# Kernel optimization log

Measured on AMD Instinct MI355X. Metric: run time of the kernel, lower is better.

Reference implementation:

```python
import jax, jax.numpy as jnp
import numpy as np

B, S, E, H, NE, K = 4, 1024, 1024, 16, 8, 2
DFF = 4 * E
DH = E // H
EPS = 1e-5


def _ln(x, g, b):
    m = jnp.mean(x, axis=-1, keepdims=True)
    v = jnp.mean(jnp.square(x - m), axis=-1, keepdims=True)
    return (x - m) * jax.lax.rsqrt(v + EPS) * g + b


def setup_inputs() -> dict:
    key = jax.random.key(0)
    ks = jax.random.split(key, 20)
    n = lambda k, sh, s: (jax.random.normal(k, sh, jnp.float32) * s)
    return {
        'x': n(ks[0], (B, S, E), 1.0),
        'ln1_g': jnp.ones((E,), jnp.float32), 'ln1_b': jnp.zeros((E,), jnp.float32),
        'wq': n(ks[1], (E, E), 0.02), 'bq': jnp.zeros((E,), jnp.float32),
        'wk': n(ks[2], (E, E), 0.02), 'bk': jnp.zeros((E,), jnp.float32),
        'wv': n(ks[3], (E, E), 0.02), 'bv': jnp.zeros((E,), jnp.float32),
        'wo': n(ks[4], (E, E), 0.02), 'bo': jnp.zeros((E,), jnp.float32),
        'ln2_g': jnp.ones((E,), jnp.float32), 'ln2_b': jnp.zeros((E,), jnp.float32),
        'sw1': n(ks[5], (E, DFF), 0.02), 'sb1': jnp.zeros((DFF,), jnp.float32),
        'sw2': n(ks[6], (DFF, E), 0.02), 'sb2': jnp.zeros((E,), jnp.float32),
        'ew1': n(ks[7], (NE, E, DFF), 0.02), 'eb1': jnp.zeros((NE, DFF), jnp.float32),
        'ew2': n(ks[8], (NE, DFF, E), 0.02), 'eb2': jnp.zeros((NE, E), jnp.float32),
        'w_gate': n(ks[9], (E, NE), 1.0),
    }


def reference(x, ln1_g, ln1_b, wq, bq, wk, bk, wv, bv, wo, bo,
              ln2_g, ln2_b, sw1, sb1, sw2, sb2, ew1, eb1, ew2, eb2, w_gate):
    # --- self-attention sublayer (eval: no dropout) ---
    res1 = x
    h = _ln(x, ln1_g, ln1_b)
    q = (h @ wq + bq).reshape(B, S, H, DH)
    k = (h @ wk + bk).reshape(B, S, H, DH)
    v = (h @ wv + bv).reshape(B, S, H, DH)
    scores = jnp.einsum('bqhd,bkhd->bhqk', q, k) / jnp.sqrt(jnp.float32(DH))
    attn = jax.nn.softmax(scores, axis=-1)
    ctx = jnp.einsum('bhqk,bkhd->bqhd', attn, v).reshape(B, S, E)
    x = res1 + (ctx @ wo + bo)

    # --- MoE sublayer ---
    res2 = x
    h2 = _ln(x, ln2_g, ln2_b)
    shared = jax.nn.gelu(h2 @ sw1 + sb1, approximate=False) @ sw2 + sb2

    # router (eval: clean logits, no noise)
    logits = h2 @ w_gate                                  # (B,S,NE)
    top_vals, top_idx = jax.lax.top_k(logits, K)          # (B,S,K)
    top_gates = jax.nn.softmax(top_vals, axis=-1)
    onehot = jax.nn.one_hot(top_idx, NE, dtype=x.dtype)   # (B,S,K,NE)
    gates = jnp.einsum('bsk,bske->bse', top_gates, onehot)
    probs = jax.nn.softmax(logits, axis=-1).reshape(-1, NE)
    P = probs.mean(0)
    f = (gates > 0).astype(x.dtype).reshape(-1, NE).mean(0)
    aux_loss = NE * jnp.sum(P * f)

    # dense all-expert compute, gated combine (matches original math)
    eh = jax.nn.gelu(jnp.einsum('bse,neh->bnsh', h2, ew1) + eb1[None, :, None, :],
                     approximate=False)
    eo = jnp.einsum('bnsh,nhe->bnse', eh, ew2) + eb2[None, :, None, :]
    expert_out = jnp.einsum('bnse,bsn->bse', eo, gates)

    return res2 + shared + expert_out, aux_loss
```

## Files before the change

### kernel.cpp

```cpp
#include <hip/hip_runtime.h>
#include <stdint.h>

#define B_    4
#define S_    1024
#define E_    1024
#define H_    16
#define NE_   8
#define DFF_  4096
#define NT_   4096
#define ROWCAP_ 9216

typedef unsigned short u16;
typedef short bf16x8 __attribute__((ext_vector_type(8)));
typedef float f32x4 __attribute__((ext_vector_type(4)));

__device__ __forceinline__ float bf2f(u16 u){ unsigned v = ((unsigned)u) << 16; return __builtin_bit_cast(float, v); }
__device__ __forceinline__ u16 f2bf(float f){ unsigned x = __builtin_bit_cast(unsigned, f); return (u16)((x + 0x7FFFu + ((x >> 16) & 1u)) >> 16); }
__device__ __forceinline__ float gelu_f(float x){ return 0.5f * x * (1.f + erff(x * 0.70710678118f)); }

__device__ __forceinline__ void gl_lds16(const u16* g, u16* l){
  __builtin_amdgcn_global_load_lds((__attribute__((address_space(1))) void*)(const_cast<u16*>(g)),
                                   (__attribute__((address_space(3))) void*)(l), 16, 0, 0);
}

__launch_bounds__(256)
__global__ void ln_kernel(const float* __restrict__ x, const float* __restrict__ g,
                          const float* __restrict__ be, u16* __restrict__ out)
{
  const int row = blockIdx.x;
  const float4 v = ((const float4*)(x + (size_t)row * E_))[threadIdx.x];
  float s = v.x + v.y + v.z + v.w;
  #pragma unroll
  for(int mm = 32; mm >= 1; mm >>= 1) s += __shfl_xor(s, mm);
  __shared__ float red[8];
  const int wid = threadIdx.x >> 6;
  if((threadIdx.x & 63) == 0) red[wid] = s;
  __syncthreads();
  const float mean = (red[0] + red[1] + red[2] + red[3]) * (1.0f / E_);
  const float d0 = v.x - mean, d1 = v.y - mean, d2 = v.z - mean, d3 = v.w - mean;
  float q2 = d0*d0 + d1*d1 + d2*d2 + d3*d3;
  #pragma unroll
  for(int mm = 32; mm >= 1; mm >>= 1) q2 += __shfl_xor(q2, mm);
  if((threadIdx.x & 63) == 0) red[4 + wid] = q2;
  __syncthreads();
  const float var = (red[4] + red[5] + red[6] + red[7]) * (1.0f / E_);
  const float rs = rsqrtf(var + 1e-5f);
  const float4 gg = ((const float4*)g)[threadIdx.x];
  const float4 bb = ((const float4*)be)[threadIdx.x];
  ushort4 o;
  o.x = f2bf(d0 * rs * gg.x + bb.x);
  o.y = f2bf(d1 * rs * gg.y + bb.y);
  o.z = f2bf(d2 * rs * gg.z + bb.z);
  o.w = f2bf(d3 * rs * gg.w + bb.w);
  ((ushort4*)(out + (size_t)row * E_))[threadIdx.x] = o;
}

__launch_bounds__(256)
__global__ void transpose_kernel(const float* __restrict__ W, u16* __restrict__ WT, int K, int N)
{
  __shared__ __align__(16) u16 t[64][72];
  const size_t zo = (size_t)blockIdx.z * K * N;
  const int k0 = blockIdx.x * 64, n0 = blockIdx.y * 64;
  const int tid = threadIdx.x;
  const int kr = tid >> 2;
  const int nc = (tid & 3) * 4;
  #pragma unroll
  for(int p = 0; p < 4; p++){
    float4 v = *(const float4*)(W + zo + (size_t)(k0 + kr) * N + n0 + nc + p * 16);
    t[nc + p*16 + 0][kr] = f2bf(v.x);
    t[nc + p*16 + 1][kr] = f2bf(v.y);
    t[nc + p*16 + 2][kr] = f2bf(v.z);
    t[nc + p*16 + 3][kr] = f2bf(v.w);
  }
  __syncthreads();
  const int nr = tid >> 3;
  const int kg = (tid & 7) * 8;
  #pragma unroll
  for(int p = 0; p < 2; p++){
    const int nn = nr + p * 32;
    unsigned u0 = t[nn][kg+0], u1 = t[nn][kg+1], u2 = t[nn][kg+2], u3 = t[nn][kg+3];
    unsigned u4 = t[nn][kg+4], u5 = t[nn][kg+5], u6 = t[nn][kg+6], u7 = t[nn][kg+7];
    uint4 o;
    o.x = u0 | (u1 << 16); o.y = u2 | (u3 << 16); o.z = u4 | (u5 << 16); o.w = u6 | (u7 << 16);
    *(uint4*)(WT + zo + (size_t)(n0 + nn) * K + k0 + kg) = o;
  }
}

template<int MODE>
__launch_bounds__(256)
__global__ void gemm_kernel(const u16* __restrict__ A, const u16* __restrict__ Bt,
                            int M, int N, int Kd,
                            const float* __restrict__ bias,
                            u16* __restrict__ outB, float* __restrict__ outF,
                            const float* __restrict__ resid)
{
  __shared__ __align__(16) u16 As[4096];
  __shared__ __align__(16) u16 Bs[4096];
  const int tid = threadIdx.x, lane = tid & 63, wid = tid >> 6;
  const int wm = wid >> 1, wn = wid & 1;
  const int tm = blockIdx.y * 128, tn = blockIdx.x * 128;

  const f32x4 zero = {0.f, 0.f, 0.f, 0.f};
  f32x4 acc[4][4];
  #pragma unroll
  for(int m = 0; m < 4; m++)
    #pragma unroll
    for(int n = 0; n < 4; n++) acc[m][n] = zero;

  const u16* gA0 = A  + (size_t)(tm + wid*32 + (lane >> 2)) * Kd + ((lane & 3) << 3);
  const u16* gA1 = gA0 + (size_t)16 * Kd;
  const u16* gB0 = Bt + (size_t)(tn + wid*32 + (lane >> 2)) * Kd + ((lane & 3) << 3);
  const u16* gB1 = gB0 + (size_t)16 * Kd;
  u16* lA0 = As + wid * 1024; u16* lA1 = lA0 + 512;
  u16* lB0 = Bs + wid * 1024; u16* lB1 = lB0 + 512;

  for(int k0 = 0; k0 < Kd; k0 += 32){
    __syncthreads();
    gl_lds16(gA0 + k0, lA0); gl_lds16(gA1 + k0, lA1);
    gl_lds16(gB0 + k0, lB0); gl_lds16(gB1 + k0, lB1);
    __syncthreads();
    bf16x8 aF[4], bF[4];
    #pragma unroll
    for(int m = 0; m < 4; m++) aF[m] = *(const bf16x8*)(As + (wm*64 + m*16 + (lane & 15)) * 32 + ((lane >> 4) << 3));
    #pragma unroll
    for(int n = 0; n < 4; n++) bF[n] = *(const bf16x8*)(Bs + (wn*64 + n*16 + (lane & 15)) * 32 + ((lane >> 4) << 3));
    #pragma unroll
    for(int m = 0; m < 4; m++)
      #pragma unroll
      for(int n = 0; n < 4; n++)
        acc[m][n] = __builtin_amdgcn_mfma_f32_16x16x32_bf16(aF[m], bF[n], acc[m][n], 0, 0, 0);
  }

  #pragma unroll
  for(int m = 0; m < 4; m++){
    const int row = tm + wm*64 + m*16 + ((lane >> 4) << 2);
    #pragma unroll
    for(int n = 0; n < 4; n++){
      const int col = tn + wn*64 + n*16 + (lane & 15);
      const float bc = bias[col];
      #pragma unroll
      for(int r = 0; r < 4; r++){
        const float v = acc[m][n][r] + bc;
        const size_t idx = (size_t)(row + r) * N + col;
        if constexpr(MODE == 0) outB[idx] = f2bf(v);
        else if constexpr(MODE == 1) outB[idx] = f2bf(gelu_f(v));
        else if constexpr(MODE == 2) outF[idx] = resid[idx] + v;
        else outF[idx] += v;
      }
    }
  }
}

__launch_bounds__(256)
__global__ void attn_kernel(const u16* __restrict__ q, const u16* __restrict__ k,
                            const u16* __restrict__ v, u16* __restrict__ ctx)
{
  __shared__ __align__(16) u16 Ks[64 * 64];
  __shared__ __align__(16) u16 Vt[64 * 72];
  __shared__ __align__(16) u16 Ps[64 * 72];
  const int tid = threadIdx.x, lane = tid & 63, wid = tid >> 6;
  const int bh = blockIdx.y, bb = bh >> 4, hh = bh & 15;
  const int q0 = blockIdx.x * 64;
  const size_t base = ((size_t)bb * S_) * E_ + hh * 64;

  bf16x8 aQ0, aQ1;
  {
    const u16* qp = q + base + (size_t)(q0 + wid*16 + (lane & 15)) * E_ + ((lane >> 4) << 3);
    aQ0 = *(const bf16x8*)qp;
    aQ1 = *(const bf16x8*)(qp + 32);
  }
  const f32x4 zero = {0.f, 0.f, 0.f, 0.f};
  f32x4 accO[4]; float mrow[4], lrow[4];
  #pragma unroll
  for(int n = 0; n < 4; n++) accO[n] = zero;
  #pragma unroll
  for(int r = 0; r < 4; r++){ mrow[r] = -1e30f; lrow[r] = 0.f; }
  const float sc = 0.125f * 1.44269504f;

  for(int kv0 = 0; kv0 < S_; kv0 += 64){
    __syncthreads();
    {
      const u16* gp = k + base + (size_t)(kv0 + wid*16 + (lane >> 3)) * E_ + ((lane & 7) << 3);
      gl_lds16(gp, Ks + (wid*16) * 64);
      gl_lds16(gp + (size_t)8 * E_, Ks + (wid*16 + 8) * 64);
    }
    {
      #pragma unroll
      for(int i = 0; i < 2; i++){
        const int tok = (tid >> 3) + i * 32;
        const int d0 = (tid & 7) << 3;
        bf16x8 vv = *(const bf16x8*)(v + base + (size_t)(kv0 + tok) * E_ + d0);
        #pragma unroll
        for(int j = 0; j < 8; j++) Vt[(d0 + j) * 72 + tok] = (u16)vv[j];
      }
    }
    __syncthreads();
    f32x4 sf[4];
    #pragma unroll
    for(int n = 0; n < 4; n++){
      bf16x8 b0 = *(const bf16x8*)(Ks + (n*16 + (lane & 15)) * 64 + ((lane >> 4) << 3));
      bf16x8 b1 = *(const bf16x8*)(Ks + (n*16 + (lane & 15)) * 64 + 32 + ((lane >> 4) << 3));
      f32x4 t = zero;
      t = __builtin_amdgcn_mfma_f32_16x16x32_bf16(aQ0, b0, t, 0, 0, 0);
      t = __builtin_amdgcn_mfma_f32_16x16x32_bf16(aQ1, b1, t, 0, 0, 0);
      sf[n] = t;
    }
    #pragma unroll
    for(int r = 0; r < 4; r++){
      const float s0 = sf[0][r]*sc, s1 = sf[1][r]*sc, s2 = sf[2][r]*sc, s3 = sf[3][r]*sc;
      float mx = fmaxf(fmaxf(s0, s1), fmaxf(s2, s3));
      #pragma unroll
      for(int mm = 1; mm < 16; mm <<= 1) mx = fmaxf(mx, __shfl_xor(mx, mm));
      const float mnew = fmaxf(mrow[r], mx);
      const float resc = exp2f(mrow[r] - mnew);
      mrow[r] = mnew;
      const float p0 = exp2f(s0 - mnew), p1 = exp2f(s1 - mnew);
      const float p2 = exp2f(s2 - mnew), p3 = exp2f(s3 - mnew);
      float ps = p0 + p1 + p2 + p3;
      #pragma unroll
      for(int mm = 1; mm < 16; mm <<= 1) ps += __shfl_xor(ps, mm);
      lrow[r] = lrow[r] * resc + ps;
      #pragma unroll
      for(int n = 0; n < 4; n++) accO[n][r] *= resc;
      const int prow = wid*16 + ((lane >> 4) << 2) + r;
      Ps[prow*72 +      (lane & 15)] = f2bf(p0);
      Ps[prow*72 + 16 + (lane & 15)] = f2bf(p1);
      Ps[prow*72 + 32 + (lane & 15)] = f2bf(p2);
      Ps[prow*72 + 48 + (lane & 15)] = f2bf(p3);
    }
    bf16x8 pa0 = *(const bf16x8*)(Ps + (wid*16 + (lane & 15)) * 72 + ((lane >> 4) << 3));
    bf16x8 pa1 = *(const bf16x8*)(Ps + (wid*16 + (lane & 15)) * 72 + 32 + ((lane >> 4) << 3));
    #pragma unroll
    for(int n = 0; n < 4; n++){
      bf16x8 b0 = *(const bf16x8*)(Vt + (n*16 + (lane & 15)) * 72 + ((lane >> 4) << 3));
      bf16x8 b1 = *(const bf16x8*)(Vt + (n*16 + (lane & 15)) * 72 + 32 + ((lane >> 4) << 3));
      accO[n] = __builtin_amdgcn_mfma_f32_16x16x32_bf16(pa0, b0, accO[n], 0, 0, 0);
      accO[n] = __builtin_amdgcn_mfma_f32_16x16x32_bf16(pa1, b1, accO[n], 0, 0, 0);
    }
  }
  #pragma unroll
  for(int n = 0; n < 4; n++)
    #pragma unroll
    for(int r = 0; r < 4; r++){
      const int row = q0 + wid*16 + ((lane >> 4) << 2) + r;
      const int col = n*16 + (lane & 15);
      ctx[base + (size_t)row * E_ + col] = f2bf(accO[n][r] / lrow[r]);
    }
}

__launch_bounds__(256)
__global__ void router_kernel(const u16* __restrict__ h2, const float* __restrict__ wg,
                              float* __restrict__ probs, float* __restrict__ tkgate,
                              int* __restrict__ tkidx, int* __restrict__ counts)
{
  const int tok = blockIdx.x * 4 + (threadIdx.x >> 6);
  const int lane = threadIdx.x & 63;
  const u16* hr = h2 + (size_t)tok * E_;
  float a0=0,a1=0,a2=0,a3=0,a4=0,a5=0,a6=0,a7=0;
  for(int i0 = lane * 8; i0 < E_; i0 += 512){
    bf16x8 hv = *(const bf16x8*)(hr + i0);
    #pragma unroll
    for(int j = 0; j < 8; j++){
      const float hx = bf2f((u16)hv[j]);
      const float* wr = wg + (size_t)(i0 + j) * NE_;
      float4 w0 = *(const float4*)wr;
      float4 w1 = *(const float4*)(wr + 4);
      a0 += hx*w0.x; a1 += hx*w0.y; a2 += hx*w0.z; a3 += hx*w0.w;
      a4 += hx*w1.x; a5 += hx*w1.y; a6 += hx*w1.z; a7 += hx*w1.w;
    }
  }
  #pragma unroll
  for(int mm = 1; mm < 64; mm <<= 1){
    a0 += __shfl_xor(a0, mm); a1 += __shfl_xor(a1, mm); a2 += __shfl_xor(a2, mm); a3 += __shfl_xor(a3, mm);
    a4 += __shfl_xor(a4, mm); a5 += __shfl_xor(a5, mm); a6 += __shfl_xor(a6, mm); a7 += __shfl_xor(a7, mm);
  }
  if(lane == 0){
    float lg[8] = {a0,a1,a2,a3,a4,a5,a6,a7};
    float mx = lg[0];
    #pragma unroll
    for(int e = 1; e < 8; e++) mx = fmaxf(mx, lg[e]);
    float se = 0.f, ex[8];
    #pragma unroll
    for(int e = 0; e < 8; e++){ ex[e] = expf(lg[e] - mx); se += ex[e]; }
    const float inv = 1.f / se;
    float* pr = probs + (size_t)tok * 8;
    #pragma unroll
    for(int e = 0; e < 8; e++) pr[e] = ex[e] * inv;
    int i1 = 0; float v1 = lg[0];
    #pragma unroll
    for(int e = 1; e < 8; e++) if(lg[e] > v1){ v1 = lg[e]; i1 = e; }
    int i2 = -1; float v2 = -3.4e38f;
    #pragma unroll
    for(int e = 0; e < 8; e++) if(e != i1 && lg[e] > v2){ v2 = lg[e]; i2 = e; }
    const float t = expf(v2 - v1);
    tkidx[tok*2] = i1; tkidx[tok*2+1] = i2;
    tkgate[tok*2] = 1.f / (1.f + t); tkgate[tok*2+1] = t / (1.f + t);
    atomicAdd(&counts[i1], 1); atomicAdd(&counts[i2], 1);
  }
}

__global__ void init_kernel(int* __restrict__ counts, int* __restrict__ rowlist)
{
  const int t = blockIdx.x * 256 + threadIdx.x;
  if(t < 16) counts[t] = 0;
  if(t < ROWCAP_) rowlist[t] = -1;
}

__global__ void scan_kernel(const int* __restrict__ counts, int* __restrict__ aoff, int* __restrict__ cursor)
{
  if(threadIdx.x == 0){
    int o = 0;
    for(int e = 0; e < 8; e++){
      aoff[e] = o; cursor[e] = o;
      o += ((counts[e] + 127) >> 7) << 7;
    }
    aoff[8] = o;
  }
}

__global__ void build_kernel(const int* __restrict__ tkidx, const float* __restrict__ tkgate,
                             int* __restrict__ cursor, int* __restrict__ rowlist, float* __restrict__ rowgate)
{
  const int t = blockIdx.x * 256 + threadIdx.x;
  if(t >= NT_) return;
  #pragma unroll
  for(int kk = 0; kk < 2; kk++){
    const int e = tkidx[t*2 + kk];
    const int pos = atomicAdd(&cursor[e], 1);
    rowlist[pos] = t; rowgate[pos] = tkgate[t*2 + kk];
  }
}

__launch_bounds__(256)
__global__ void egemm1_kernel(const u16* __restrict__ Ah2, const u16* __restrict__ ewT,
                              const float* __restrict__ eb1,
                              const int* __restrict__ rowlist, const int* __restrict__ aoff,
                              u16* __restrict__ ehid)
{
  const int rowTile = blockIdx.y * 128;
  if(rowTile >= aoff[8]) return;
  int e = 0;
  #pragma unroll
  for(int i = 1; i < 8; i++) if(rowTile >= aoff[i]) e = i;
  __shared__ __align__(16) u16 As[4096];
  __shared__ __align__(16) u16 Bs[4096];
  const int tid = threadIdx.x, lane = tid & 63, wid = tid >> 6;
  const int wm = wid >> 1, wn = wid & 1;
  const int tn = blockIdx.x * 128;
  const u16* Bt = ewT + (size_t)e * DFF_ * E_;

  const int r0 = rowTile + wid*32 + (lane >> 2);
  int t0 = rowlist[r0];      if(t0 < 0) t0 = 0;
  int t1 = rowlist[r0 + 16]; if(t1 < 0) t1 = 0;
  const u16* gA0 = Ah2 + (size_t)t0 * E_ + ((lane & 3) << 3);
  const u16* gA1 = Ah2 + (size_t)t1 * E_ + ((lane & 3) << 3);
  const u16* gB0 = Bt + (size_t)(tn + wid*32 + (lane >> 2)) * E_ + ((lane & 3) << 3);
  const u16* gB1 = gB0 + (size_t)16 * E_;
  u16* lA0 = As + wid*1024; u16* lA1 = lA0 + 512;
  u16* lB0 = Bs + wid*1024; u16* lB1 = lB0 + 512;

  const f32x4 zero = {0.f,0.f,0.f,0.f};
  f32x4 acc[4][4];
  #pragma unroll
  for(int m = 0; m < 4; m++)
    #pragma unroll
    for(int n = 0; n < 4; n++) acc[m][n] = zero;

  for(int k0 = 0; k0 < E_; k0 += 32){
    __syncthreads();
    gl_lds16(gA0 + k0, lA0); gl_lds16(gA1 + k0, lA1);
    gl_lds16(gB0 + k0, lB0); gl_lds16(gB1 + k0, lB1);
    __syncthreads();
    bf16x8 aF[4], bF[4];
    #pragma unroll
    for(int m = 0; m < 4; m++) aF[m] = *(const bf16x8*)(As + (wm*64 + m*16 + (lane & 15)) * 32 + ((lane >> 4) << 3));
    #pragma unroll
    for(int n = 0; n < 4; n++) bF[n] = *(const bf16x8*)(Bs + (wn*64 + n*16 + (lane & 15)) * 32 + ((lane >> 4) << 3));
    #pragma unroll
    for(int m = 0; m < 4; m++)
      #pragma unroll
      for(int n = 0; n < 4; n++)
        acc[m][n] = __builtin_amdgcn_mfma_f32_16x16x32_bf16(aF[m], bF[n], acc[m][n], 0, 0, 0);
  }
  #pragma unroll
  for(int m = 0; m < 4; m++){
    const int row = rowTile + wm*64 + m*16 + ((lane >> 4) << 2);
    #pragma unroll
    for(int n = 0; n < 4; n++){
      const int col = tn + wn*64 + n*16 + (lane & 15);
      const float bc = eb1[e * DFF_ + col];
      #pragma unroll
      for(int r = 0; r < 4; r++)
        ehid[(size_t)(row + r) * DFF_ + col] = f2bf(gelu_f(acc[m][n][r] + bc));
    }
  }
}

__launch_bounds__(256)
__global__ void egemm2_kernel(const u16* __restrict__ ehid, const u16* __restrict__ ewT2,
                              const float* __restrict__ eb2,
                              const int* __restrict__ rowlist, const float* __restrict__ rowgate,
                              const int* __restrict__ aoff, float* __restrict__ outF)
{
  const int rowTile = blockIdx.y * 128;
  if(rowTile >= aoff[8]) return;
  int e = 0;
  #pragma unroll
  for(int i = 1; i < 8; i++) if(rowTile >= aoff[i]) e = i;
  __shared__ __align__(16) u16 As[4096];
  __shared__ __align__(16) u16 Bs[4096];
  const int tid = threadIdx.x, lane = tid & 63, wid = tid >> 6;
  const int wm = wid >> 1, wn = wid & 1;
  const int tn = blockIdx.x * 128;
  const u16* Bt = ewT2 + (size_t)e * E_ * DFF_;

  const u16* gA0 = ehid + (size_t)(rowTile + wid*32 + (lane >> 2)) * DFF_ + ((lane & 3) << 3);
  const u16* gA1 = gA0 + (size_t)16 * DFF_;
  const u16* gB0 = Bt + (size_t)(tn + wid*32 + (lane >> 2)) * DFF_ + ((lane & 3) << 3);
  const u16* gB1 = gB0 + (size_t)16 * DFF_;
  u16* lA0 = As + wid*1024; u16* lA1 = lA0 + 512;
  u16* lB0 = Bs + wid*1024; u16* lB1 = lB0 + 512;

  const f32x4 zero = {0.f,0.f,0.f,0.f};
  f32x4 acc[4][4];
  #pragma unroll
  for(int m = 0; m < 4; m++)
    #pragma unroll
    for(int n = 0; n < 4; n++) acc[m][n] = zero;

  for(int k0 = 0; k0 < DFF_; k0 += 32){
    __syncthreads();
    gl_lds16(gA0 + k0, lA0); gl_lds16(gA1 + k0, lA1);
    gl_lds16(gB0 + k0, lB0); gl_lds16(gB1 + k0, lB1);
    __syncthreads();
    bf16x8 aF[4], bF[4];
    #pragma unroll
    for(int m = 0; m < 4; m++) aF[m] = *(const bf16x8*)(As + (wm*64 + m*16 + (lane & 15)) * 32 + ((lane >> 4) << 3));
    #pragma unroll
    for(int n = 0; n < 4; n++) bF[n] = *(const bf16x8*)(Bs + (wn*64 + n*16 + (lane & 15)) * 32 + ((lane >> 4) << 3));
    #pragma unroll
    for(int m = 0; m < 4; m++)
      #pragma unroll
      for(int n = 0; n < 4; n++)
        acc[m][n] = __builtin_amdgcn_mfma_f32_16x16x32_bf16(aF[m], bF[n], acc[m][n], 0, 0, 0);
  }
  #pragma unroll
  for(int m = 0; m < 4; m++){
    const int row = rowTile + wm*64 + m*16 + ((lane >> 4) << 2);
    #pragma unroll
    for(int r = 0; r < 4; r++){
      const int rr = row + r;
      const int tok = rowlist[rr];
      if(tok < 0) continue;
      const float g = rowgate[rr];
      #pragma unroll
      for(int n = 0; n < 4; n++){
        const int col = tn + wn*64 + n*16 + (lane & 15);
        atomicAdd(&outF[(size_t)tok * E_ + col], g * (acc[m][n][r] + eb2[e * E_ + col]));
      }
    }
  }
}

__launch_bounds__(256)
__global__ void aux_kernel(const float* __restrict__ probs, const int* __restrict__ counts,
                           float* __restrict__ outaux)
{
  float a[8];
  #pragma unroll
  for(int e = 0; e < 8; e++) a[e] = 0.f;
  for(int t = threadIdx.x; t < NT_; t += 256){
    const float* p = probs + (size_t)t * 8;
    #pragma unroll
    for(int e = 0; e < 8; e++) a[e] += p[e];
  }
  #pragma unroll
  for(int mm = 1; mm < 64; mm <<= 1)
    #pragma unroll
    for(int e = 0; e < 8; e++) a[e] += __shfl_xor(a[e], mm);
  __shared__ float part[4][8];
  const int wid = threadIdx.x >> 6;
  if((threadIdx.x & 63) == 0)
    for(int e = 0; e < 8; e++) part[wid][e] = a[e];
  __syncthreads();
  if(threadIdx.x == 0){
    float aux = 0.f;
    for(int e = 0; e < 8; e++){
      const float P = (part[0][e] + part[1][e] + part[2][e] + part[3][e]) / (float)NT_;
      const float f = (float)counts[e] / (float)NT_;
      aux += P * f;
    }
    outaux[0] = (float)NE_ * aux;
  }
}

extern "C" void kernel_launch(void* const* d_in, const int* in_sizes, int n_in,
                              void* d_out, int out_size, void* d_ws, size_t ws_size,
                              hipStream_t stream)
{
  (void)in_sizes; (void)n_in; (void)out_size; (void)ws_size;
  const float* x    = (const float*)d_in[0];
  const float* ln1g = (const float*)d_in[1];
  const float* ln1b = (const float*)d_in[2];
  const float* wq   = (const float*)d_in[3];
  const float* bq   = (const float*)d_in[4];
  const float* wk   = (const float*)d_in[5];
  const float* bk   = (const float*)d_in[6];
  const float* wv   = (const float*)d_in[7];
  const float* bv   = (const float*)d_in[8];
  const float* wo   = (const float*)d_in[9];
  const float* bo   = (const float*)d_in[10];
  const float* ln2g = (const float*)d_in[11];
  const float* ln2b = (const float*)d_in[12];
  const float* sw1  = (const float*)d_in[13];
  const float* sb1  = (const float*)d_in[14];
  const float* sw2  = (const float*)d_in[15];
  const float* sb2  = (const float*)d_in[16];
  const float* ew1  = (const float*)d_in[17];
  const float* eb1  = (const float*)d_in[18];
  const float* ew2  = (const float*)d_in[19];
  const float* eb2  = (const float*)d_in[20];
  const float* wgate= (const float*)d_in[21];
  float* out = (float*)d_out;
  char* ws = (char*)d_ws;

  const size_t MB = 1024ull * 1024ull;
  u16* h     = (u16*)(ws + 0);
  u16* h2    = (u16*)(ws + 8*MB);
  u16* wT    = (u16*)(ws + 16*MB);
  char* rt   = ws + 24*MB;
  float* probs   = (float*)(rt);
  float* tkgate  = (float*)(rt + 128*1024);
  int*   tkidx   = (int*)  (rt + 160*1024);
  int*   counts  = (int*)  (rt + 192*1024);
  int*   aoff    = (int*)  (rt + 192*1024 + 64);
  int*   cursor  = (int*)  (rt + 192*1024 + 128);
  int*   rowlist = (int*)  (rt + 256*1024);
  float* rowgate = (float*)(rt + 296*1024);
  u16* qb    = (u16*)(ws + 32*MB);
  u16* kb    = (u16*)(ws + 40*MB);
  u16* vb    = (u16*)(ws + 48*MB);
  u16* ctx   = (u16*)(ws + 56*MB);
  u16* hidS  = (u16*)(ws + 64*MB);
  u16* ewT   = (u16*)(ws + 32*MB);
  u16* ehid  = (u16*)(ws + 96*MB);

  ln_kernel<<<NT_, 256, 0, stream>>>(x, ln1g, ln1b, h);
  transpose_kernel<<<dim3(16,16,1), 256, 0, stream>>>(wq, wT,                 E_, E_);
  transpose_kernel<<<dim3(16,16,1), 256, 0, stream>>>(wk, wT + 1024*1024,     E_, E_);
  transpose_kernel<<<dim3(16,16,1), 256, 0, stream>>>(wv, wT + 2*1024*1024,   E_, E_);
  gemm_kernel<0><<<dim3(8,32), 256, 0, stream>>>(h, wT,               NT_, E_, E_, bq, qb, nullptr, nullptr);
  gemm_kernel<0><<<dim3(8,32), 256, 0, stream>>>(h, wT + 1024*1024,   NT_, E_, E_, bk, kb, nullptr, nullptr);
  gemm_kernel<0><<<dim3(8,32), 256, 0, stream>>>(h, wT + 2*1024*1024, NT_, E_, E_, bv, vb, nullptr, nullptr);
  attn_kernel<<<dim3(16,64), 256, 0, stream>>>(qb, kb, vb, ctx);
  transpose_kernel<<<dim3(16,16,1), 256, 0, stream>>>(wo, wT, E_, E_);
  gemm_kernel<2><<<dim3(8,32), 256, 0, stream>>>(ctx, wT, NT_, E_, E_, bo, nullptr, out, x);

  ln_kernel<<<NT_, 256, 0, stream>>>(out, ln2g, ln2b, h2);
  transpose_kernel<<<dim3(16,64,1), 256, 0, stream>>>(sw1, wT, E_, DFF_);
  gemm_kernel<1><<<dim3(32,32), 256, 0, stream>>>(h2, wT, NT_, DFF_, E_, sb1, hidS, nullptr, nullptr);
  transpose_kernel<<<dim3(64,16,1), 256, 0, stream>>>(sw2, wT, DFF_, E_);
  gemm_kernel<3><<<dim3(8,32), 256, 0, stream>>>(hidS, wT, NT_, E_, DFF_, sb2, nullptr, out, nullptr);

  init_kernel<<<36, 256, 0, stream>>>(counts, rowlist);
  router_kernel<<<1024, 256, 0, stream>>>(h2, wgate, probs, tkgate, tkidx, counts);
  scan_kernel<<<1, 64, 0, stream>>>(counts, aoff, cursor);
  build_kernel<<<16, 256, 0, stream>>>(tkidx, tkgate, cursor, rowlist, rowgate);

  transpose_kernel<<<dim3(16,64,8), 256, 0, stream>>>(ew1, ewT, E_, DFF_);
  egemm1_kernel<<<dim3(32,72), 256, 0, stream>>>(h2, ewT, eb1, rowlist, aoff, ehid);
  transpose_kernel<<<dim3(64,16,8), 256, 0, stream>>>(ew2, ewT, DFF_, E_);
  egemm2_kernel<<<dim3(8,72), 256, 0, stream>>>(ehid, ewT, eb2, rowlist, rowgate, aoff, out);

  aux_kernel<<<1, 256, 0, stream>>>(probs, counts, out + (size_t)NT_ * E_);
}
```

Baseline: 909.1 us.

## Fuse QKV projections into one GEMM and split-K narrow GEMMs with atomics

```diff
diff --git a/kernel.cpp b/kernel.cpp
--- a/kernel.cpp
+++ b/kernel.cpp
@@ -8,6 +8,7 @@
 #define NE_   8
 #define DFF_  4096
 #define NT_   4096
+#define QS_   3072
 #define ROWCAP_ 9216
 
 typedef unsigned short u16;
@@ -25,10 +26,12 @@
 
 __launch_bounds__(256)
 __global__ void ln_kernel(const float* __restrict__ x, const float* __restrict__ g,
-                          const float* __restrict__ be, u16* __restrict__ out)
+                          const float* __restrict__ be, u16* __restrict__ out,
+                          float* __restrict__ xcopy)
 {
   const int row = blockIdx.x;
   const float4 v = ((const float4*)(x + (size_t)row * E_))[threadIdx.x];
+  if(xcopy) ((float4*)(xcopy + (size_t)row * E_))[threadIdx.x] = v;
   float s = v.x + v.y + v.z + v.w;
   #pragma unroll
   for(int mm = 32; mm >= 1; mm >>= 1) s += __shfl_xor(s, mm);
@@ -86,19 +89,28 @@
   }
 }
 
+__global__ void bcat_kernel(const float* __restrict__ bq, const float* __restrict__ bk,
+                            const float* __restrict__ bv, float* __restrict__ bcat)
+{
+  const int i = blockIdx.x * 256 + threadIdx.x;
+  if(i < 1024) bcat[i] = bq[i];
+  else if(i < 2048) bcat[i] = bk[i - 1024];
+  else if(i < 3072) bcat[i] = bv[i - 2048];
+}
+
 template<int MODE>
 __launch_bounds__(256)
 __global__ void gemm_kernel(const u16* __restrict__ A, const u16* __restrict__ Bt,
-                            int M, int N, int Kd,
-                            const float* __restrict__ bias,
-                            u16* __restrict__ outB, float* __restrict__ outF,
-                            const float* __restrict__ resid)
+                            int N, int Kfull, int kLen,
+                            const float* __restrict__ bias, float bscale,
+                            u16* __restrict__ outB, float* __restrict__ outF)
 {
   __shared__ __align__(16) u16 As[4096];
   __shared__ __align__(16) u16 Bs[4096];
   const int tid = threadIdx.x, lane = tid & 63, wid = tid >> 6;
   const int wm = wid >> 1, wn = wid & 1;
   const int tm = blockIdx.y * 128, tn = blockIdx.x * 128;
+  const int kOff = blockIdx.z * kLen;
 
   const f32x4 zero = {0.f, 0.f, 0.f, 0.f};
   f32x4 acc[4][4];
@@ -107,14 +119,14 @@
     #pragma unroll
     for(int n = 0; n < 4; n++) acc[m][n] = zero;
 
-  const u16* gA0 = A  + (size_t)(tm + wid*32 + (lane >> 2)) * Kd + ((lane & 3) << 3);
-  const u16* gA1 = gA0 + (size_t)16 * Kd;
-  const u16* gB0 = Bt + (size_t)(tn + wid*32 + (lane >> 2)) * Kd + ((lane & 3) << 3);
-  const u16* gB1 = gB0 + (size_t)16 * Kd;
+  const u16* gA0 = A  + (size_t)(tm + wid*32 + (lane >> 2)) * Kfull + ((lane & 3) << 3);
+  const u16* gA1 = gA0 + (size_t)16 * Kfull;
+  const u16* gB0 = Bt + (size_t)(tn + wid*32 + (lane >> 2)) * Kfull + ((lane & 3) << 3);
+  const u16* gB1 = gB0 + (size_t)16 * Kfull;
   u16* lA0 = As + wid * 1024; u16* lA1 = lA0 + 512;
   u16* lB0 = Bs + wid * 1024; u16* lB1 = lB0 + 512;
 
-  for(int k0 = 0; k0 < Kd; k0 += 32){
+  for(int k0 = kOff; k0 < kOff + kLen; k0 += 32){
     __syncthreads();
     gl_lds16(gA0 + k0, lA0); gl_lds16(gA1 + k0, lA1);
     gl_lds16(gB0 + k0, lB0); gl_lds16(gB1 + k0, lB1);
@@ -137,23 +149,21 @@
     #pragma unroll
     for(int n = 0; n < 4; n++){
       const int col = tn + wn*64 + n*16 + (lane & 15);
-      const float bc = bias[col];
+      const float bc = bias[col] * bscale;
       #pragma unroll
       for(int r = 0; r < 4; r++){
         const float v = acc[m][n][r] + bc;
         const size_t idx = (size_t)(row + r) * N + col;
         if constexpr(MODE == 0) outB[idx] = f2bf(v);
         else if constexpr(MODE == 1) outB[idx] = f2bf(gelu_f(v));
-        else if constexpr(MODE == 2) outF[idx] = resid[idx] + v;
-        else outF[idx] += v;
+        else atomicAdd(&outF[idx], v);
       }
     }
   }
 }
 
 __launch_bounds__(256)
-__global__ void attn_kernel(const u16* __restrict__ q, const u16* __restrict__ k,
-                            const u16* __restrict__ v, u16* __restrict__ ctx)
+__global__ void attn_kernel(const u16* __restrict__ qkv, u16* __restrict__ ctx)
 {
   __shared__ __align__(16) u16 Ks[64 * 64];
   __shared__ __align__(16) u16 Vt[64 * 72];
@@ -161,11 +171,12 @@
   const int tid = threadIdx.x, lane = tid & 63, wid = tid >> 6;
   const int bh = blockIdx.y, bb = bh >> 4, hh = bh & 15;
   const int q0 = blockIdx.x * 64;
-  const size_t base = ((size_t)bb * S_) * E_ + hh * 64;
+  const size_t tok0 = (size_t)bb * S_;
+  const int hcol = hh * 64;
 
   bf16x8 aQ0, aQ1;
   {
-    const u16* qp = q + base + (size_t)(q0 + wid*16 + (lane & 15)) * E_ + ((lane >> 4) << 3);
+    const u16* qp = qkv + (tok0 + q0 + wid*16 + (lane & 15)) * QS_ + hcol + ((lane >> 4) << 3);
     aQ0 = *(const bf16x8*)qp;
     aQ1 = *(const bf16x8*)(qp + 32);
   }
@@ -180,16 +191,16 @@
   for(int kv0 = 0; kv0 < S_; kv0 += 64){
     __syncthreads();
     {
-      const u16* gp = k + base + (size_t)(kv0 + wid*16 + (lane >> 3)) * E_ + ((lane & 7) << 3);
+      const u16* gp = qkv + (tok0 + kv0 + wid*16 + (lane >> 3)) * QS_ + 1024 + hcol + ((lane & 7) << 3);
       gl_lds16(gp, Ks + (wid*16) * 64);
-      gl_lds16(gp + (size_t)8 * E_, Ks + (wid*16 + 8) * 64);
+      gl_lds16(gp + (size_t)8 * QS_, Ks + (wid*16 + 8) * 64);
     }
     {
       #pragma unroll
       for(int i = 0; i < 2; i++){
         const int tok = (tid >> 3) + i * 32;
         const int d0 = (tid & 7) << 3;
-        bf16x8 vv = *(const bf16x8*)(v + base + (size_t)(kv0 + tok) * E_ + d0);
+        bf16x8 vv = *(const bf16x8*)(qkv + (tok0 + kv0 + tok) * QS_ + 2048 + hcol + d0);
         #pragma unroll
         for(int j = 0; j < 8; j++) Vt[(d0 + j) * 72 + tok] = (u16)vv[j];
       }
@@ -238,13 +249,14 @@
       accO[n] = __builtin_amdgcn_mfma_f32_16x16x32_bf16(pa1, b1, accO[n], 0, 0, 0);
     }
   }
+  const size_t cbase = tok0 * E_ + hcol;
   #pragma unroll
   for(int n = 0; n < 4; n++)
     #pragma unroll
     for(int r = 0; r < 4; r++){
       const int row = q0 + wid*16 + ((lane >> 4) << 2) + r;
       const int col = n*16 + (lane & 15);
-      ctx[base + (size_t)row * E_ + col] = f2bf(accO[n][r] / lrow[r]);
+      ctx[cbase + (size_t)row * E_ + col] = f2bf(accO[n][r] / lrow[r]);
     }
 }
 
@@ -412,6 +424,7 @@
   const int tid = threadIdx.x, lane = tid & 63, wid = tid >> 6;
   const int wm = wid >> 1, wn = wid & 1;
   const int tn = blockIdx.x * 128;
+  const int kOff = blockIdx.z * 1024;
   const u16* Bt = ewT2 + (size_t)e * E_ * DFF_;
 
   const u16* gA0 = ehid + (size_t)(rowTile + wid*32 + (lane >> 2)) * DFF_ + ((lane & 3) << 3);
@@ -428,7 +441,7 @@
     #pragma unroll
     for(int n = 0; n < 4; n++) acc[m][n] = zero;
 
-  for(int k0 = 0; k0 < DFF_; k0 += 32){
+  for(int k0 = kOff; k0 < kOff + 1024; k0 += 32){
     __syncthreads();
     gl_lds16(gA0 + k0, lA0); gl_lds16(gA1 + k0, lA1);
     gl_lds16(gB0 + k0, lB0); gl_lds16(gB1 + k0, lB1);
@@ -456,7 +469,7 @@
       #pragma unroll
       for(int n = 0; n < 4; n++){
         const int col = tn + wn*64 + n*16 + (lane & 15);
-        atomicAdd(&outF[(size_t)tok * E_ + col], g * (acc[m][n][r] + eb2[e * E_ + col]));
+        atomicAdd(&outF[(size_t)tok * E_ + col], g * (acc[m][n][r] + eb2[e * E_ + col] * 0.25f));
       }
     }
   }
@@ -537,30 +550,28 @@
   int*   cursor  = (int*)  (rt + 192*1024 + 128);
   int*   rowlist = (int*)  (rt + 256*1024);
   float* rowgate = (float*)(rt + 296*1024);
-  u16* qb    = (u16*)(ws + 32*MB);
-  u16* kb    = (u16*)(ws + 40*MB);
-  u16* vb    = (u16*)(ws + 48*MB);
+  float* bcat    = (float*)(rt + 512*1024);
+  u16* qkvb  = (u16*)(ws + 32*MB);
   u16* ctx   = (u16*)(ws + 56*MB);
   u16* hidS  = (u16*)(ws + 64*MB);
   u16* ewT   = (u16*)(ws + 32*MB);
   u16* ehid  = (u16*)(ws + 96*MB);
 
-  ln_kernel<<<NT_, 256, 0, stream>>>(x, ln1g, ln1b, h);
+  ln_kernel<<<NT_, 256, 0, stream>>>(x, ln1g, ln1b, h, out);
+  bcat_kernel<<<12, 256, 0, stream>>>(bq, bk, bv, bcat);
   transpose_kernel<<<dim3(16,16,1), 256, 0, stream>>>(wq, wT,                 E_, E_);
   transpose_kernel<<<dim3(16,16,1), 256, 0, stream>>>(wk, wT + 1024*1024,     E_, E_);
   transpose_kernel<<<dim3(16,16,1), 256, 0, stream>>>(wv, wT + 2*1024*1024,   E_, E_);
-  gemm_kernel<0><<<dim3(8,32), 256, 0, stream>>>(h, wT,               NT_, E_, E_, bq, qb, nullptr, nullptr);
-  gemm_kernel<0><<<dim3(8,32), 256, 0, stream>>>(h, wT + 1024*1024,   NT_, E_, E_, bk, kb, nullptr, nullptr);
-  gemm_kernel<0><<<dim3(8,32), 256, 0, stream>>>(h, wT + 2*1024*1024, NT_, E_, E_, bv, vb, nullptr, nullptr);
-  attn_kernel<<<dim3(16,64), 256, 0, stream>>>(qb, kb, vb, ctx);
+  gemm_kernel<0><<<dim3(24,32,1), 256, 0, stream>>>(h, wT, QS_, E_, E_, bcat, 1.f, qkvb, nullptr);
+  attn_kernel<<<dim3(16,64), 256, 0, stream>>>(qkvb, ctx);
   transpose_kernel<<<dim3(16,16,1), 256, 0, stream>>>(wo, wT, E_, E_);
-  gemm_kernel<2><<<dim3(8,32), 256, 0, stream>>>(ctx, wT, NT_, E_, E_, bo, nullptr, out, x);
-
-  ln_kernel<<<NT_, 256, 0, stream>>>(out, ln2g, ln2b, h2);
+  gemm_kernel<4><<<dim3(8,32,4), 256, 0, stream>>>(ctx, wT, E_, E_, 256, bo, 0.25f, nullptr, out);
+
+  ln_kernel<<<NT_, 256, 0, stream>>>(out, ln2g, ln2b, h2, nullptr);
   transpose_kernel<<<dim3(16,64,1), 256, 0, stream>>>(sw1, wT, E_, DFF_);
-  gemm_kernel<1><<<dim3(32,32), 256, 0, stream>>>(h2, wT, NT_, DFF_, E_, sb1, hidS, nullptr, nullptr);
+  gemm_kernel<1><<<dim3(32,32,1), 256, 0, stream>>>(h2, wT, DFF_, E_, E_, sb1, 1.f, hidS, nullptr);
   transpose_kernel<<<dim3(64,16,1), 256, 0, stream>>>(sw2, wT, DFF_, E_);
-  gemm_kernel<3><<<dim3(8,32), 256, 0, stream>>>(hidS, wT, NT_, E_, DFF_, sb2, nullptr, out, nullptr);
+  gemm_kernel<4><<<dim3(8,32,4), 256, 0, stream>>>(hidS, wT, E_, DFF_, 1024, sb2, 0.25f, nullptr, out);
 
   init_kernel<<<36, 256, 0, stream>>>(counts, rowlist);
   router_kernel<<<1024, 256, 0, stream>>>(h2, wgate, probs, tkgate, tkidx, counts);
@@ -570,7 +581,7 @@
   transpose_kernel<<<dim3(16,64,8), 256, 0, stream>>>(ew1, ewT, E_, DFF_);
   egemm1_kernel<<<dim3(32,72), 256, 0, stream>>>(h2, ewT, eb1, rowlist, aoff, ehid);
   transpose_kernel<<<dim3(64,16,8), 256, 0, stream>>>(ew2, ewT, DFF_, E_);
-  egemm2_kernel<<<dim3(8,72), 256, 0, stream>>>(ehid, ewT, eb2, rowlist, rowgate, aoff, out);
+  egemm2_kernel<<<dim3(8,72,4), 256, 0, stream>>>(ehid, ewT, eb2, rowlist, rowgate, aoff, out);
 
   aux_kernel<<<1, 256, 0, stream>>>(probs, counts, out + (size_t)NT_ * E_);
 }
```

Measured after the change: 964.1 us. 6.1% more time.
